# Kernel optimization log

Measured on AMD Instinct MI355X. Metric: run time of the kernel, lower is better.

## Reference

```python
import jax, jax.numpy as jnp
import numpy as np

B, T, F = 256, 196, 263
H = 1024  # LSTM hidden size; lin1/lin_text each produce H//2


def setup_inputs() -> dict:
    key = jax.random.key(0)
    ks = jax.random.split(key, 12)
    s = lambda k, shp, fan: jax.random.normal(k, shp, jnp.float32) / np.sqrt(fan)
    return {
        "motions": jax.random.normal(ks[0], (B, T, F), jnp.float32),
        "text_embedding": jax.random.normal(ks[1], (B, 768), jnp.float32),
        "lin_text_w": s(ks[2], (H // 2, 768), 768),
        "lin_text_b": jnp.zeros((H // 2,), jnp.float32),
        "lin1_w": s(ks[3], (H // 2, F), F),
        "lin1_b": jnp.zeros((H // 2,), jnp.float32),
        "w_ih": s(ks[4], (4 * H, H), H),
        "w_hh": s(ks[5], (4 * H, H), H),
        "b_ih": s(ks[6], (4 * H,), H),
        "b_hh": s(ks[7], (4 * H,), H),
        "lin2_w": s(ks[8], (F, H), H),
        "lin2_b": jnp.zeros((F,), jnp.float32),
    }


def reference(motions, text_embedding, lin_text_w, lin_text_b, lin1_w, lin1_b,
              w_ih, w_hh, b_ih, b_hh, lin2_w, lin2_b):
    batch, seq_len, _ = motions.shape
    hid = w_hh.shape[1]
    # pooled BERT embedding -> hidden/2 (lin_text); computed once outside the loop
    text_emb = text_embedding @ lin_text_w.T + lin_text_b  # [B, H/2]
    b_gates = b_ih + b_hh  # [4H]

    def step(carry, _):
        h, c, frame = carry
        enc = frame @ lin1_w.T + lin1_b                      # [B, H/2]
        x = jnp.concatenate([enc, text_emb], axis=-1)        # [B, H]
        gates = x @ w_ih.T + h @ w_hh.T + b_gates            # [B, 4H]
        i, f, g, o = jnp.split(gates, 4, axis=-1)            # torch LSTMCell gate order
        c = jax.nn.sigmoid(f) * c + jax.nn.sigmoid(i) * jnp.tanh(g)
        h = jax.nn.sigmoid(o) * jnp.tanh(c)
        out = h @ lin2_w.T + lin2_b                          # [B, F]
        new_frame = frame + out                              # method='current_frame' residual
        return (h, c, new_frame), new_frame

    h0 = jnp.zeros((batch, hid), motions.dtype)
    c0 = jnp.zeros((batch, hid), motions.dtype)
    frame0 = motions[:, 0, :]
    _, outs = jax.lax.scan(step, (h0, c0, frame0), None, length=seq_len)
    return jnp.transpose(outs, (1, 0, 2))  # [B, T, F]
```

## Files before the change

kernel.cpp:

```cpp
#include <hip/hip_runtime.h>
#include <math.h>

typedef _Float16 f16;
typedef __attribute__((ext_vector_type(8))) _Float16 f16x8;
typedef __attribute__((ext_vector_type(4))) float f32x4;

#define Bsz 256
#define Tsz 196
#define Fsz 263
#define TFs (Tsz*Fsz)
#define SX  1312
#define KCH 41
#define LOSC 2048.0f
#define LOINV 0.00048828125f

#define OFF_WALLHI 0u
#define OFF_WALLLO 10747904u
#define OFF_R1     21495808u
#define OFF_R2     26214400u
#define OFF_XHI0   26214400u
#define OFF_XLO0   26886144u
#define OFF_XHI1   27557888u
#define OFF_XLO1   28229632u
#define OFF_PROJ   28901376u
#define OFF_CGP    30408704u
#define OFF_L2PH   34603008u
#define OFF_L2PL   35258368u
#define OFF_LIN1T  35913728u
#define OFF_LTWT   36452352u
#define OFF_TEXTE  38025216u
#define OFF_BIASG  38549504u
#define OFF_WCT    38565888u
#define WS_BYTES   43284480u

__device__ __forceinline__ void glds16(const void* g, void* l) {
    __builtin_amdgcn_global_load_lds(
        (const __attribute__((address_space(1))) void*)g,
        (__attribute__((address_space(3))) void*)l, 16, 0, 0);
}
__device__ __forceinline__ float sigm(float x) { return 1.f / (1.f + expf(-x)); }
__device__ __forceinline__ void split16(float x, f16& hi, f16& lo) {
    hi = (f16)x;
    lo = (f16)((x - (float)hi) * LOSC);
}
#define MFMA16(a,b,c) __builtin_amdgcn_mfma_f32_16x16x32_f16(a,b,c,0,0,0)

#define WAIT_BAR(N) do { \
    asm volatile("s_waitcnt vmcnt(" #N ")" ::: "memory"); \
    __builtin_amdgcn_s_barrier(); \
    __builtin_amdgcn_sched_barrier(0); \
} while (0)

__global__ __launch_bounds__(256) void tpose(const float* __restrict__ src,
                                             float* __restrict__ dst, int M, int N) {
    __shared__ float tile[32][33];
    int bx = blockIdx.x, by = blockIdx.y;
    int tx = threadIdx.x & 31, ty = threadIdx.x >> 5;
#pragma unroll
    for (int i = 0; i < 4; ++i) {
        int row = by*32 + ty*4 + i, col = bx*32 + tx;
        tile[ty*4+i][tx] = (row < M && col < N) ? src[(size_t)row*N + col] : 0.f;
    }
    __syncthreads();
#pragma unroll
    for (int i = 0; i < 4; ++i) {
        int row = bx*32 + ty*4 + i, col = by*32 + tx;
        if (row < N && col < M) dst[(size_t)row*M + col] = tile[tx][ty*4+i];
    }
}

__global__ __launch_bounds__(256) void biasg_k(const float* __restrict__ bih,
                                               const float* __restrict__ bhh,
                                               const float* __restrict__ l1b,
                                               const float* __restrict__ wih,
                                               float* __restrict__ bg) {
    int j = blockIdx.x*4 + (threadIdx.x >> 6);
    int l = threadIdx.x & 63;
    const float* wr = wih + (size_t)j*1024 + l*8;
    const float* lb = l1b + l*8;
    float s = 0.f;
#pragma unroll
    for (int e = 0; e < 8; ++e) s += lb[e] * wr[e];
#pragma unroll
    for (int off = 32; off; off >>= 1) s += __shfl_down(s, off, 64);
    if (l == 0) bg[j] = bih[j] + bhh[j] + s;
}

__global__ __launch_bounds__(256) void nn_gemm(const float* __restrict__ A,
                                               const float* __restrict__ B,
                                               const float* __restrict__ bias,
                                               float* __restrict__ C,
                                               int M, int MA, int N, int K) {
    __shared__ float As[32][33];
    __shared__ float Bs[32][64];
    int tid = threadIdx.x;
    int r0 = blockIdx.y*32, c0 = blockIdx.x*64;
    int tr = tid >> 4, tc = tid & 15;
    float acc[2][4] = {};
    for (int k0 = 0; k0 < K; k0 += 32) {
        int m = tid >> 3, kb = (tid & 7)*4;
        int row = r0 + m;
#pragma unroll
        for (int i = 0; i < 4; ++i)
            As[m][kb+i] = (row < MA) ? A[(size_t)row*K + k0 + kb + i] : 0.f;
#pragma unroll
        for (int i = 0; i < 8; ++i) {
            int fi = i*256 + tid, kk = fi >> 6, cc = fi & 63;
            Bs[kk][cc] = B[(size_t)(k0+kk)*N + c0 + cc];
        }
        __syncthreads();
#pragma unroll
        for (int k = 0; k < 32; ++k) {
            float a0 = As[2*tr][k], a1 = As[2*tr+1][k];
            float b0 = Bs[k][4*tc], b1 = Bs[k][4*tc+1], b2 = Bs[k][4*tc+2], b3 = Bs[k][4*tc+3];
            acc[0][0]+=a0*b0; acc[0][1]+=a0*b1; acc[0][2]+=a0*b2; acc[0][3]+=a0*b3;
            acc[1][0]+=a1*b0; acc[1][1]+=a1*b1; acc[1][2]+=a1*b2; acc[1][3]+=a1*b3;
        }
        __syncthreads();
    }
#pragma unroll
    for (int i = 0; i < 2; ++i) {
        int row = r0 + 2*tr + i;
        if (row < M)
#pragma unroll
            for (int j = 0; j < 4; ++j) {
                int col = c0 + 4*tc + j;
                C[(size_t)row*N + col] = acc[i][j] + (bias ? bias[col] : 0.f);
            }
    }
}

__global__ __launch_bounds__(256) void pack_wall(const float* __restrict__ WcT,
                                                 const float* __restrict__ whh,
                                                 f16* __restrict__ Wh,
                                                 f16* __restrict__ Wl) {
    int q = threadIdx.x;
    int ct = blockIdx.x, kc = blockIdx.y;
    int k = kc*32 + (((q&3) ^ ((q>>3)&3)) << 3);
    int p = ct*64 + (q>>2);
    int j = (p&3)*1024 + (p>>2);
    size_t ob = ((size_t)(kc*64 + ct)*256 + q)*8;
#pragma unroll
    for (int e = 0; e < 8; ++e) {
        int kk = k + e;
        float v = (kk < 288) ? WcT[(size_t)j*288 + kk]
                             : whh[(size_t)j*1024 + (kk - 288)];
        split16(v, Wh[ob+e], Wl[ob+e]);
    }
}

__global__ __launch_bounds__(256) void pack_lin2(const float* __restrict__ l2w,
                                                 f16* __restrict__ Lh,
                                                 f16* __restrict__ Ll) {
    int q = threadIdx.x;
    int ct = blockIdx.x, kc = blockIdx.y;
    int k = kc*32 + (((q&3) ^ ((q>>3)&3)) << 3);
    int f = ct*64 + (q>>2);
    size_t ob = ((size_t)(kc*5 + ct)*256 + q)*8;
#pragma unroll
    for (int e = 0; e < 8; ++e) {
        float v = (f < Fsz) ? l2w[(size_t)f*1024 + k + e] : 0.f;
        split16(v, Lh[ob+e], Ll[ob+e]);
    }
}

__global__ __launch_bounds__(256) void permute_cg(const float* __restrict__ cj,
                                                  float* __restrict__ cp) {
    int idx = blockIdx.x*256 + threadIdx.x;
    int b = idx >> 12, p = idx & 4095;
    cp[idx] = cj[(b << 12) + ((p & 3) << 10) + (p >> 2)];
}

__global__ __launch_bounds__(256) void init_k(const float* __restrict__ motions,
                                              f16* __restrict__ Xh0,
                                              f16* __restrict__ Xl0,
                                              float* __restrict__ cSt) {
    int idx = blockIdx.x*256 + threadIdx.x;
    if (idx < 256*SX) {
        int b = idx / SX, k = idx - b*SX;
        float v = (k < Fsz) ? motions[(size_t)b*TFs + k] : 0.f;
        split16(v, Xh0[idx], Xl0[idx]);
    } else {
        int i2 = idx - 256*SX;
        if (i2 < 256*1024) cSt[i2] = 0.f;
    }
}

__global__ __launch_bounds__(256) void k1_gates(
        const f16* __restrict__ Xh, const f16* __restrict__ Xl,
        const f16* __restrict__ Wh, const f16* __restrict__ Wl,
        const float* __restrict__ cgp, float* __restrict__ cSt,
        f16* __restrict__ XhN, f16* __restrict__ XlN)
{
    __shared__ __attribute__((aligned(16))) char smem[65536];
    const int tid = threadIdx.x;
    const int ct = blockIdx.x, rt = blockIdx.y;
    const int r0 = rt*64, p0 = ct*64;
    const int l = tid & 63;
    const int wr = (tid >> 7) & 1, wc = (tid >> 6) & 1;

    const int aswz = (((tid&3) ^ ((tid>>3)&3)) << 3);
    const f16* aSrcH = Xh + (size_t)(r0 + (tid>>2))*SX + aswz;
    const f16* aSrcL = Xl + (size_t)(r0 + (tid>>2))*SX + aswz;
    const f16* bSrcH = Wh + (size_t)ct*2048 + tid*8;
    const f16* bSrcL = Wl + (size_t)ct*2048 + tid*8;

    int offA[2], offB[2];
#pragma unroll
    for (int R = 0; R < 2; ++R) {
        int g = l >> 4;
        int row = wr*32 + R*16 + (l & 15);
        offA[R] = row*64 + ((g ^ ((row>>1)&3)) & 3)*16;
        int col = wc*32 + R*16 + (l & 15);
        offB[R] = col*64 + ((g ^ ((col>>1)&3)) & 3)*16;
    }
    f32x4 hh[2][2] = {}, hl[2][2] = {}, lh[2][2] = {};

    auto issueLoads = [&](int c) {
        const int buf = c & 3;
        char* dA = smem + buf*8192 + tid*16;
        char* dB = smem + 32768 + buf*8192 + tid*16;
        glds16(aSrcH + c*32, dA);
        glds16(aSrcL + c*32, dA + 4096);
        glds16(bSrcH + (size_t)c*131072, dB);
        glds16(bSrcL + (size_t)c*131072, dB + 4096);
    };
    auto compute = [&](int c) {
        const char* At = smem + (c & 3)*8192;
        const char* Bt = smem + 32768 + (c & 3)*8192;
        f16x8 ah[2], al[2], bh[2], bl[2];
#pragma unroll
        for (int R = 0; R < 2; ++R) {
            ah[R] = *(const f16x8*)(At + offA[R]);
            al[R] = *(const f16x8*)(At + 4096 + offA[R]);
            bh[R] = *(const f16x8*)(Bt + offB[R]);
            bl[R] = *(const f16x8*)(Bt + 4096 + offB[R]);
        }
#pragma unroll
        for (int R = 0; R < 2; ++R)
#pragma unroll
            for (int C = 0; C < 2; ++C) {
                hh[R][C] = MFMA16(ah[R], bh[C], hh[R][C]);
                hl[R][C] = MFMA16(ah[R], bl[C], hl[R][C]);
                lh[R][C] = MFMA16(al[R], bh[C], lh[R][C]);
            }
    };

    issueLoads(0); issueLoads(1); issueLoads(2);
#pragma unroll 1
    for (int c = 0; c < KCH-3; ++c) {
        WAIT_BAR(8);
        issueLoads(c+3);
        compute(c);
    }
    WAIT_BAR(8); compute(KCH-3);
    WAIT_BAR(4); compute(KCH-2);
    WAIT_BAR(0); compute(KCH-1);
    __syncthreads();

    float* gl = (float*)smem;
#pragma unroll
    for (int R = 0; R < 2; ++R)
#pragma unroll
        for (int C = 0; C < 2; ++C) {
            f32x4 d = hh[R][C] + (hl[R][C] + lh[R][C]) * LOINV;
            int col = wc*32 + C*16 + (l & 15);
            int rb = wr*32 + R*16 + ((l >> 4) << 2);
#pragma unroll
            for (int j = 0; j < 4; ++j) {
                int r = rb + j;
                gl[r*64 + (col ^ ((r & 7) << 2))] = d[j];
            }
        }
    __syncthreads();
#pragma unroll
    for (int q = 0; q < 4; ++q) {
        int s = q*256 + tid;
        int m = s >> 4, u = s & 15;
        f32x4 gt = *(const f32x4*)(gl + m*64 + ((u << 2) ^ ((m & 7) << 2)));
        f32x4 cg = *(const f32x4*)(cgp + (size_t)(r0 + m)*4096 + p0 + (u << 2));
        float gi = gt.x + cg.x, gf = gt.y + cg.y, gg = gt.z + cg.z, go = gt.w + cg.w;
        int ug = ct*16 + u;
        int ci = (r0 + m)*1024 + ug;
        float cO = cSt[ci];
        float cN = sigm(gf)*cO + sigm(gi)*tanhf(gg);
        float hN = sigm(go)*tanhf(cN);
        cSt[ci] = cN;
        split16(hN, XhN[(size_t)(r0 + m)*SX + 288 + ug], XlN[(size_t)(r0 + m)*SX + 288 + ug]);
    }
}

__global__ __launch_bounds__(256) void k3_proj(
        const f16* __restrict__ Xh, const f16* __restrict__ Xl,
        const f16* __restrict__ Lh, const f16* __restrict__ Ll,
        float* __restrict__ proj)
{
    __shared__ __attribute__((aligned(16))) char smem[65536];
    const int tid = threadIdx.x;
    const int ct = blockIdx.x, rt = blockIdx.y, ks = blockIdx.z;
    const int r0 = rt*64;
    const int l = tid & 63;
    const int wr = (tid >> 7) & 1, wc = (tid >> 6) & 1;

    const int aswz = (((tid&3) ^ ((tid>>3)&3)) << 3);
    const f16* aSrcH = Xh + (size_t)(r0 + (tid>>2))*SX + 288 + aswz + ks*256;
    const f16* aSrcL = Xl + (size_t)(r0 + (tid>>2))*SX + 288 + aswz + ks*256;
    const f16* bSrcH = Lh + (size_t)(ks*8)*10240 + (size_t)ct*2048 + tid*8;
    const f16* bSrcL = Ll + (size_t)(ks*8)*10240 + (size_t)ct*2048 + tid*8;

    int offA[2], offB[2];
#pragma unroll
    for (int R = 0; R < 2; ++R) {
        int g = l >> 4;
        int row = wr*32 + R*16 + (l & 15);
        offA[R] = row*64 + ((g ^ ((row>>1)&3)) & 3)*16;
        int col = wc*32 + R*16 + (l & 15);
        offB[R] = col*64 + ((g ^ ((col>>1)&3)) & 3)*16;
    }
    f32x4 hh[2][2] = {}, hl[2][2] = {}, lh[2][2] = {};

    auto issueLoads = [&](int c) {
        const int buf = c & 3;
        char* dA = smem + buf*8192 + tid*16;
        char* dB = smem + 32768 + buf*8192 + tid*16;
        glds16(aSrcH + c*32, dA);
        glds16(aSrcL + c*32, dA + 4096);
        glds16(bSrcH + (size_t)c*10240, dB);
        glds16(bSrcL + (size_t)c*10240, dB + 4096);
    };
    auto compute = [&](int c) {
        const char* At = smem + (c & 3)*8192;
        const char* Bt = smem + 32768 + (c & 3)*8192;
        f16x8 ah[2], al[2], bh[2], bl[2];
#pragma unroll
        for (int R = 0; R < 2; ++R) {
            ah[R] = *(const f16x8*)(At + offA[R]);
            al[R] = *(const f16x8*)(At + 4096 + offA[R]);
            bh[R] = *(const f16x8*)(Bt + offB[R]);
            bl[R] = *(const f16x8*)(Bt + 4096 + offB[R]);
        }
#pragma unroll
        for (int R = 0; R < 2; ++R)
#pragma unroll
            for (int C = 0; C < 2; ++C) {
                hh[R][C] = MFMA16(ah[R], bh[C], hh[R][C]);
                hl[R][C] = MFMA16(ah[R], bl[C], hl[R][C]);
                lh[R][C] = MFMA16(al[R], bh[C], lh[R][C]);
            }
    };

    issueLoads(0); issueLoads(1); issueLoads(2);
#pragma unroll 1
    for (int c = 0; c < 5; ++c) {
        WAIT_BAR(8);
        issueLoads(c+3);
        compute(c);
    }
    WAIT_BAR(8); compute(5);
    WAIT_BAR(4); compute(6);
    WAIT_BAR(0); compute(7);

    float* pout = proj + (size_t)ks*81920;
#pragma unroll
    for (int R = 0; R < 2; ++R)
#pragma unroll
        for (int C = 0; C < 2; ++C) {
            f32x4 d = hh[R][C] + (hl[R][C] + lh[R][C]) * LOINV;
            int col = ct*64 + wc*32 + C*16 + (l & 15);
            int rb = r0 + wr*32 + R*16 + ((l >> 4) << 2);
#pragma unroll
            for (int j = 0; j < 4; ++j)
                pout[(size_t)(rb + j)*320 + col] = d[j];
        }
}

__global__ __launch_bounds__(256) void k2b(const float* __restrict__ fprev,
                                           const float* __restrict__ proj,
                                           const float* __restrict__ l2b,
                                           float* __restrict__ outT,
                                           f16* __restrict__ XhN,
                                           f16* __restrict__ XlN) {
    int idx = blockIdx.x*256 + threadIdx.x;
    if (idx >= 256*288) return;
    int b = idx / 288, f = idx - b*288;
    if (f < Fsz) {
        float v = fprev[(size_t)b*TFs + f] + l2b[f];
#pragma unroll
        for (int ks = 0; ks < 4; ++ks) v += proj[(size_t)ks*81920 + b*320 + f];
        outT[(size_t)b*TFs + f] = v;
        split16(v, XhN[(size_t)b*SX + f], XlN[(size_t)b*SX + f]);
    } else {
        XhN[(size_t)b*SX + f] = (f16)0.f;
        XlN[(size_t)b*SX + f] = (f16)0.f;
    }
}

extern "C" void kernel_launch(void* const* d_in, const int* in_sizes, int n_in,
                              void* d_out_v, int out_size, void* d_ws, size_t ws_size,
                              hipStream_t stream) {
    const float* motions = (const float*)d_in[0];
    const float* temb    = (const float*)d_in[1];
    const float* ltw     = (const float*)d_in[2];
    const float* ltb     = (const float*)d_in[3];
    const float* l1w     = (const float*)d_in[4];
    const float* l1b     = (const float*)d_in[5];
    const float* wih     = (const float*)d_in[6];
    const float* whh     = (const float*)d_in[7];
    const float* bih     = (const float*)d_in[8];
    const float* bhh     = (const float*)d_in[9];
    const float* l2w     = (const float*)d_in[10];
    const float* l2b     = (const float*)d_in[11];
    float* out = (float*)d_out_v;
    char* ws = (char*)d_ws;
    if (ws_size < (size_t)WS_BYTES) return;

    f16*   WallHi = (f16*)(ws + OFF_WALLHI);
    f16*   WallLo = (f16*)(ws + OFF_WALLLO);
    float* WihT   = (float*)(ws + OFF_WALLHI);
    float* Wcomb  = (float*)(ws + OFF_R1);
    float* cSt    = (float*)(ws + OFF_R1);
    float* cgj    = (float*)(ws + OFF_R2);
    f16*   XhB[2] = { (f16*)(ws + OFF_XHI0), (f16*)(ws + OFF_XHI1) };
    f16*   XlB[2] = { (f16*)(ws + OFF_XLO0), (f16*)(ws + OFF_XLO1) };
    float* proj   = (float*)(ws + OFF_PROJ);
    float* cgp    = (float*)(ws + OFF_CGP);
    f16*   L2h    = (f16*)(ws + OFF_L2PH);
    f16*   L2l    = (f16*)(ws + OFF_L2PL);
    float* lin1t  = (float*)(ws + OFF_LIN1T);
    float* ltwT   = (float*)(ws + OFF_LTWT);
    float* textE  = (float*)(ws + OFF_TEXTE);
    float* biasG  = (float*)(ws + OFF_BIASG);
    float* WcT    = (float*)(ws + OFF_WCT);

    dim3 blk(256);
    tpose<<<dim3(32,128), blk, 0, stream>>>(wih, WihT, 4096, 1024);
    tpose<<<dim3(24, 16), blk, 0, stream>>>(ltw, ltwT, 512, 768);
    tpose<<<dim3( 9, 16), blk, 0, stream>>>(l1w, lin1t, 512, 263);
    biasg_k<<<1024, blk, 0, stream>>>(bih, bhh, l1b, wih, biasG);
    nn_gemm<<<dim3( 8, 8), blk, 0, stream>>>(temb, ltwT, ltb, textE, 256, 256, 512, 768);
    nn_gemm<<<dim3(64, 9), blk, 0, stream>>>(lin1t, WihT, nullptr, Wcomb, 288, 263, 4096, 512);
    nn_gemm<<<dim3(64, 8), blk, 0, stream>>>(textE, WihT + (size_t)512*4096, biasG, cgj,
                                             256, 256, 4096, 512);
    tpose<<<dim3(128, 9), blk, 0, stream>>>(Wcomb, WcT, 288, 4096);
    permute_cg<<<4096, blk, 0, stream>>>(cgj, cgp);
    pack_wall<<<dim3(64, 41), blk, 0, stream>>>(WcT, whh, WallHi, WallLo);
    pack_lin2<<<dim3(5, 32), blk, 0, stream>>>(l2w, L2h, L2l);
    init_k<<<2336, blk, 0, stream>>>(motions, XhB[0], XlB[0], cSt);

    for (int t = 0; t < Tsz; ++t) {
        f16* Xhc = XhB[t & 1],      *Xlc = XlB[t & 1];
        f16* Xhn = XhB[(t+1) & 1],  *Xln = XlB[(t+1) & 1];
        const float* fprev = (t == 0) ? motions : (out + (size_t)(t-1)*Fsz);
        k1_gates<<<dim3(64, 4), blk, 0, stream>>>(Xhc, Xlc, WallHi, WallLo,
                                                  cgp, cSt, Xhn, Xln);
        k3_proj<<<dim3(5, 4, 4), blk, 0, stream>>>(Xhn, Xln, L2h, L2l, proj);
        k2b<<<288, blk, 0, stream>>>(fprev, proj, l2b, out + (size_t)t*Fsz, Xhn, Xln);
    }
}
```

Measured before the change: 4.665 ms.

## Fuse split-K reduction into k3_proj via atomic last-block counter

Removes the separate k2b launch per timestep by having the last of the four split-K blocks for each output tile (found through an atomic counter in workspace) sum the partial projections, add bias and residual, write the output and repack the next input. This saves one kernel launch and its dependency gap on each of the 196 steps. In exchange it adds atomics, fences and a serialized tail in one block per tile. The LDS buffer layout is also interleaved so each stage's A and B tiles sit next to each other.

```diff
diff --git a/kernel.cpp b/kernel.cpp
--- a/kernel.cpp
+++ b/kernel.cpp
@@ -31,7 +31,8 @@
 #define OFF_TEXTE  38025216u
 #define OFF_BIASG  38549504u
 #define OFF_WCT    38565888u
-#define WS_BYTES   43284480u
+#define OFF_CTR    43284480u
+#define WS_BYTES   43284560u
 
 __device__ __forceinline__ void glds16(const void* g, void* l) {
     __builtin_amdgcn_global_load_lds(
@@ -44,7 +45,6 @@
     lo = (f16)((x - (float)hi) * LOSC);
 }
 #define MFMA16(a,b,c) __builtin_amdgcn_mfma_f32_16x16x32_f16(a,b,c,0,0,0)
-
 #define WAIT_BAR(N) do { \
     asm volatile("s_waitcnt vmcnt(" #N ")" ::: "memory"); \
     __builtin_amdgcn_s_barrier(); \
@@ -174,15 +174,17 @@
 __global__ __launch_bounds__(256) void init_k(const float* __restrict__ motions,
                                               f16* __restrict__ Xh0,
                                               f16* __restrict__ Xl0,
-                                              float* __restrict__ cSt) {
+                                              float* __restrict__ cSt,
+                                              unsigned* __restrict__ ctr) {
     int idx = blockIdx.x*256 + threadIdx.x;
     if (idx < 256*SX) {
         int b = idx / SX, k = idx - b*SX;
         float v = (k < Fsz) ? motions[(size_t)b*TFs + k] : 0.f;
         split16(v, Xh0[idx], Xl0[idx]);
-    } else {
-        int i2 = idx - 256*SX;
-        if (i2 < 256*1024) cSt[i2] = 0.f;
+    } else if (idx < 256*SX + 262144) {
+        cSt[idx - 256*SX] = 0.f;
+    } else if (idx < 256*SX + 262144 + 20) {
+        ctr[idx - 256*SX - 262144] = 0u;
     }
 }
 
@@ -293,9 +295,14 @@
 __global__ __launch_bounds__(256) void k3_proj(
         const f16* __restrict__ Xh, const f16* __restrict__ Xl,
         const f16* __restrict__ Lh, const f16* __restrict__ Ll,
-        float* __restrict__ proj)
+        float* __restrict__ proj,
+        const float* __restrict__ fprev, const float* __restrict__ l2b,
+        float* __restrict__ outT,
+        f16* __restrict__ XhN, f16* __restrict__ XlN,
+        unsigned* __restrict__ ctr)
 {
     __shared__ __attribute__((aligned(16))) char smem[65536];
+    __shared__ unsigned lastFlag;
     const int tid = threadIdx.x;
     const int ct = blockIdx.x, rt = blockIdx.y, ks = blockIdx.z;
     const int r0 = rt*64;
@@ -321,16 +328,16 @@
 
     auto issueLoads = [&](int c) {
         const int buf = c & 3;
-        char* dA = smem + buf*8192 + tid*16;
-        char* dB = smem + 32768 + buf*8192 + tid*16;
+        char* dA = smem + buf*16384 + tid*16;
+        char* dB = smem + buf*16384 + 8192 + tid*16;
         glds16(aSrcH + c*32, dA);
         glds16(aSrcL + c*32, dA + 4096);
         glds16(bSrcH + (size_t)c*10240, dB);
         glds16(bSrcL + (size_t)c*10240, dB + 4096);
     };
     auto compute = [&](int c) {
-        const char* At = smem + (c & 3)*8192;
-        const char* Bt = smem + 32768 + (c & 3)*8192;
+        const char* At = smem + (c & 3)*16384;
+        const char* Bt = smem + (c & 3)*16384 + 8192;
         f16x8 ah[2], al[2], bh[2], bl[2];
 #pragma unroll
         for (int R = 0; R < 2; ++R) {
@@ -372,26 +379,42 @@
             for (int j = 0; j < 4; ++j)
                 pout[(size_t)(rb + j)*320 + col] = d[j];
         }
-}
-
-__global__ __launch_bounds__(256) void k2b(const float* __restrict__ fprev,
-                                           const float* __restrict__ proj,
-                                           const float* __restrict__ l2b,
-                                           float* __restrict__ outT,
-                                           f16* __restrict__ XhN,
-                                           f16* __restrict__ XlN) {
-    int idx = blockIdx.x*256 + threadIdx.x;
-    if (idx >= 256*288) return;
-    int b = idx / 288, f = idx - b*288;
-    if (f < Fsz) {
-        float v = fprev[(size_t)b*TFs + f] + l2b[f];
-#pragma unroll
-        for (int ks = 0; ks < 4; ++ks) v += proj[(size_t)ks*81920 + b*320 + f];
-        outT[(size_t)b*TFs + f] = v;
-        split16(v, XhN[(size_t)b*SX + f], XlN[(size_t)b*SX + f]);
-    } else {
-        XhN[(size_t)b*SX + f] = (f16)0.f;
-        XlN[(size_t)b*SX + f] = (f16)0.f;
+
+    __syncthreads();
+    if (tid == 0) {
+        __builtin_amdgcn_fence(__ATOMIC_RELEASE, "agent");
+        unsigned old = __hip_atomic_fetch_add(&ctr[rt*5 + ct], 1u,
+                                              __ATOMIC_ACQ_REL, __HIP_MEMORY_SCOPE_AGENT);
+        lastFlag = old;
+        if (old == 3u)
+            __hip_atomic_store(&ctr[rt*5 + ct], 0u, __ATOMIC_RELAXED,
+                               __HIP_MEMORY_SCOPE_AGENT);
+    }
+    __syncthreads();
+    if (lastFlag != 3u) return;
+    __builtin_amdgcn_fence(__ATOMIC_ACQUIRE, "agent");
+
+#pragma unroll 1
+    for (int idx = tid; idx < 4096; idx += 256) {
+        int r = idx >> 6, cc = idx & 63;
+        int b = r0 + r;
+        int f = ct*64 + cc;
+        if (f < 288) {
+            size_t xo = (size_t)b*SX + f;
+            if (f < Fsz) {
+                size_t po = (size_t)b*320 + f;
+                float s = proj[po] + proj[81920 + po] + proj[163840 + po] + proj[245760 + po];
+                float v = fprev[(size_t)b*TFs + f] + l2b[f] + s;
+                outT[(size_t)b*TFs + f] = v;
+                f16 hi, lo;
+                split16(v, hi, lo);
+                XhN[xo] = hi;
+                XlN[xo] = lo;
+            } else {
+                XhN[xo] = (f16)0.f;
+                XlN[xo] = (f16)0.f;
+            }
+        }
     }
 }
 
@@ -414,23 +437,24 @@
     char* ws = (char*)d_ws;
     if (ws_size < (size_t)WS_BYTES) return;
 
-    f16*   WallHi = (f16*)(ws + OFF_WALLHI);
-    f16*   WallLo = (f16*)(ws + OFF_WALLLO);
-    float* WihT   = (float*)(ws + OFF_WALLHI);
-    float* Wcomb  = (float*)(ws + OFF_R1);
-    float* cSt    = (float*)(ws + OFF_R1);
-    float* cgj    = (float*)(ws + OFF_R2);
-    f16*   XhB[2] = { (f16*)(ws + OFF_XHI0), (f16*)(ws + OFF_XHI1) };
-    f16*   XlB[2] = { (f16*)(ws + OFF_XLO0), (f16*)(ws + OFF_XLO1) };
-    float* proj   = (float*)(ws + OFF_PROJ);
-    float* cgp    = (float*)(ws + OFF_CGP);
-    f16*   L2h    = (f16*)(ws + OFF_L2PH);
-    f16*   L2l    = (f16*)(ws + OFF_L2PL);
-    float* lin1t  = (float*)(ws + OFF_LIN1T);
-    float* ltwT   = (float*)(ws + OFF_LTWT);
-    float* textE  = (float*)(ws + OFF_TEXTE);
-    float* biasG  = (float*)(ws + OFF_BIASG);
-    float* WcT    = (float*)(ws + OFF_WCT);
+    f16*      WallHi = (f16*)(ws + OFF_WALLHI);
+    f16*      WallLo = (f16*)(ws + OFF_WALLLO);
+    float*    cSt    = (float*)(ws + OFF_R1);
+    f16*      XhB[2] = { (f16*)(ws + OFF_XHI0), (f16*)(ws + OFF_XHI1) };
+    f16*      XlB[2] = { (f16*)(ws + OFF_XLO0), (f16*)(ws + OFF_XLO1) };
+    float*    proj   = (float*)(ws + OFF_PROJ);
+    float*    cgp    = (float*)(ws + OFF_CGP);
+    f16*      L2h    = (f16*)(ws + OFF_L2PH);
+    f16*      L2l    = (f16*)(ws + OFF_L2PL);
+    unsigned* ctr    = (unsigned*)(ws + OFF_CTR);
+    float* WihT  = (float*)(ws + OFF_WALLHI);
+    float* Wcomb = (float*)(ws + OFF_R1);
+    float* cgj   = (float*)(ws + OFF_R2);
+    float* lin1t = (float*)(ws + OFF_LIN1T);
+    float* ltwT  = (float*)(ws + OFF_LTWT);
+    float* textE = (float*)(ws + OFF_TEXTE);
+    float* biasG = (float*)(ws + OFF_BIASG);
+    float* WcT   = (float*)(ws + OFF_WCT);
 
     dim3 blk(256);
     tpose<<<dim3(32,128), blk, 0, stream>>>(wih, WihT, 4096, 1024);
@@ -445,7 +469,7 @@
     permute_cg<<<4096, blk, 0, stream>>>(cgj, cgp);
     pack_wall<<<dim3(64, 41), blk, 0, stream>>>(WcT, whh, WallHi, WallLo);
     pack_lin2<<<dim3(5, 32), blk, 0, stream>>>(l2w, L2h, L2l);
-    init_k<<<2336, blk, 0, stream>>>(motions, XhB[0], XlB[0], cSt);
+    init_k<<<2337, blk, 0, stream>>>(motions, XhB[0], XlB[0], cSt, ctr);
 
     for (int t = 0; t < Tsz; ++t) {
         f16* Xhc = XhB[t & 1],      *Xlc = XlB[t & 1];
@@ -453,7 +477,8 @@
         const float* fprev = (t == 0) ? motions : (out + (size_t)(t-1)*Fsz);
         k1_gates<<<dim3(64, 4), blk, 0, stream>>>(Xhc, Xlc, WallHi, WallLo,
                                                   cgp, cSt, Xhn, Xln);
-        k3_proj<<<dim3(5, 4, 4), blk, 0, stream>>>(Xhn, Xln, L2h, L2l, proj);
-        k2b<<<288, blk, 0, stream>>>(fprev, proj, l2b, out + (size_t)t*Fsz, Xhn, Xln);
-    }
-}
+        k3_proj<<<dim3(5, 4, 4), blk, 0, stream>>>(Xhn, Xln, L2h, L2l, proj,
+                                                   fprev, l2b, out + (size_t)t*Fsz,
+                                                   Xhn, Xln, ctr);
+    }
+}
```

Result: slower. 6.789 ms (+45.5%).
